# Kernel optimization log

Measured on AMD Instinct MI355X. Metric: run time of the kernel, lower is better.

The kernel has to match this reference:

```python
import jax, jax.numpy as jnp
import numpy as np

N_NODES = 100000
N_EDGES = 1600000
IN_C, HID_C, OUT_C = 128, 128, 64


def setup_inputs() -> dict:
    key = jax.random.key(0)
    ks = jax.random.split(key, 6)
    x = jax.random.normal(ks[0], (N_NODES, IN_C), dtype=jnp.float32)
    edge_index = jax.random.randint(ks[1], (2, N_EDGES), 0, N_NODES)
    W1 = jax.random.normal(ks[2], (IN_C, HID_C), dtype=jnp.float32) * (1.0 / np.sqrt(IN_C))
    b1 = jnp.zeros((HID_C,), dtype=jnp.float32)
    W2 = jax.random.normal(ks[3], (HID_C, OUT_C), dtype=jnp.float32) * (1.0 / np.sqrt(HID_C))
    b2 = jnp.zeros((OUT_C,), dtype=jnp.float32)
    return {"x": x, "edge_index": edge_index, "W1": W1, "b1": b1, "W2": W2, "b2": b2}


def gcn_conv(x, W, b, src, dst):
    # PyG GCNConv: D^{-1/2} (A + I) D^{-1/2} X W + b, with self-loops handled
    # analytically (no explicit self-loop edges materialized).
    h = x @ W                                             # [N, d_out]
    ones = jnp.ones(src.shape[0], dtype=h.dtype)
    deg = jax.ops.segment_sum(ones, dst, num_segments=N_NODES) + 1.0  # +1 self-loop
    dinv = jax.lax.rsqrt(deg)                             # deg >= 1, safe
    norm = dinv[src] * dinv[dst]                          # [E]
    msg = h[src] * norm[:, None]                          # gather + scale  [E, d_out]
    agg = jax.ops.segment_sum(msg, dst, num_segments=N_NODES)
    agg = agg + h * (dinv * dinv)[:, None]                # self-loop contribution
    return agg + b


def reference(x, edge_index, W1, b1, W2, b2):
    src, dst = edge_index[0], edge_index[1]
    h = jax.nn.relu(gcn_conv(x, W1, b1, src, dst))
    # dropout is identity in eval mode
    out = gcn_conv(h, W2, b2, src, dst)
    return out
```

## Files before the change

kernel.cpp:

```cpp
#include <hip/hip_runtime.h>

#define N_NODESC 100000
#define N_EDGESC 1600000
#define NB_BUCKETS 391
#define BUCKET_CAP 5120
#define CHUNK_A 2048
#define NBKT_BLOCKS ((N_EDGESC + CHUNK_A - 1) / CHUNK_A)

typedef __attribute__((ext_vector_type(4))) float floatx4;
typedef __attribute__((ext_vector_type(8))) short shortx8;

__device__ __forceinline__ unsigned short f32_to_bf16_rne(float f) {
    unsigned int u = __float_as_uint(f);
    unsigned int r = u + 0x7fffu + ((u >> 16) & 1u);
    return (unsigned short)(r >> 16);
}
__device__ __forceinline__ float bf16_to_f32(unsigned short h) {
    return __uint_as_float(((unsigned int)h) << 16);
}
__device__ __forceinline__ float bflo(unsigned int u) { return __uint_as_float(u << 16); }
__device__ __forceinline__ float bfhi(unsigned int u) { return __uint_as_float(u & 0xffff0000u); }
__device__ __forceinline__ unsigned int pack2bf(float a, float b) {
    return ((unsigned int)f32_to_bf16_rne(b) << 16) | (unsigned int)f32_to_bf16_rne(a);
}

__global__ __launch_bounds__(256) void k_wfrag_all(const float* __restrict__ W1,
        const float* __restrict__ W2,
        unsigned short* __restrict__ w1hi, unsigned short* __restrict__ w1lo,
        unsigned short* __restrict__ w2hi, unsigned short* __restrict__ w2lo,
        int* __restrict__ gcur) {
    int t = threadIdx.x;
    if (blockIdx.x == 0)
        for (int i = t; i < NB_BUCKETS; i += 256) gcur[i] = i * BUCKET_CAP;
    int idx = blockIdx.x * 256 + t;
    float f;
    int k, col, C, o;
    unsigned short *phi, *plo;
    if (idx < 16384) {
        k = idx >> 7; col = idx & 127; C = 8;
        f = W1[idx]; phi = w1hi; plo = w1lo;
    } else {
        int idx2 = idx - 16384;
        k = idx2 >> 6; col = idx2 & 63; C = 4;
        f = W2[idx2]; phi = w2hi; plo = w2lo;
    }
    unsigned short hi = f32_to_bf16_rne(f);
    unsigned short lo = f32_to_bf16_rne(f - bf16_to_f32(hi));
    int kc = k >> 5, q = (k >> 3) & 3, j = k & 7;
    int c = col >> 4, n = col & 15;
    o = (((kc * C + c) * 4 + q) * 16 + n) * 8 + j;
    phi[o] = hi; plo[o] = lo;
}

__global__ __launch_bounds__(256) void k_fusedA(const float* __restrict__ x,
        const unsigned short* __restrict__ w1hi, const unsigned short* __restrict__ w1lo,
        const int* __restrict__ src, const int* __restrict__ dst,
        int* __restrict__ gcur, unsigned int* __restrict__ tmp,
        unsigned short* __restrict__ H) {
    __shared__ __align__(16) float etile[4][16][132];
    if (blockIdx.x < NBKT_BLOCKS) {
        int* hist = (int*)etile;
        int t = threadIdx.x;
        for (int i = t; i < NB_BUCKETS; i += 256) hist[i] = 0;
        __syncthreads();
        int base = blockIdx.x * CHUNK_A;
        int end = min(base + CHUNK_A, N_EDGESC);
        for (int e = base + t; e < end; e += 256)
            atomicAdd(&hist[dst[e] >> 8], 1);
        __syncthreads();
        for (int i = t; i < NB_BUCKETS; i += 256) {
            int c = hist[i];
            hist[i] = (c > 0) ? atomicAdd(&gcur[i], c) : 0;
        }
        __syncthreads();
        for (int e = base + t; e < end; e += 256) {
            int d = dst[e];
            int pos = atomicAdd(&hist[d >> 8], 1);
            tmp[pos] = ((unsigned int)src[e] << 8) | (unsigned int)(d & 255);
        }
        return;
    }
    int wv = threadIdx.x >> 6, lane = threadIdx.x & 63;
    int n16 = lane & 15, q = lane >> 4;
    int rowBase = (blockIdx.x - NBKT_BLOCKS) * 128 + wv * 32;
    floatx4 acc[2][8];
#pragma unroll
    for (int m = 0; m < 2; ++m)
#pragma unroll
        for (int c = 0; c < 8; ++c) acc[m][c] = (floatx4){0.f, 0.f, 0.f, 0.f};

    const shortx8* whi8 = (const shortx8*)w1hi;
    const shortx8* wlo8 = (const shortx8*)w1lo;

    for (int kc = 0; kc < 4; ++kc) {
        shortx8 ahi[2], alo[2];
#pragma unroll
        for (int m = 0; m < 2; ++m) {
            int r = rowBase + m * 16 + n16;
            if (r >= N_NODESC) r = N_NODESC - 1;
            const float* xp = &x[(size_t)r * 128 + kc * 32 + q * 8];
            floatx4 x0 = *(const floatx4*)xp;
            floatx4 x1 = *(const floatx4*)(xp + 4);
#pragma unroll
            for (int jj = 0; jj < 4; ++jj) {
                unsigned short h0 = f32_to_bf16_rne(x0[jj]);
                ahi[m][jj] = (short)h0;
                alo[m][jj] = (short)f32_to_bf16_rne(x0[jj] - bf16_to_f32(h0));
                unsigned short h1 = f32_to_bf16_rne(x1[jj]);
                ahi[m][jj + 4] = (short)h1;
                alo[m][jj + 4] = (short)f32_to_bf16_rne(x1[jj] - bf16_to_f32(h1));
            }
        }
#pragma unroll
        for (int c = 0; c < 8; ++c) {
            int fo = (kc * 8 + c) * 64 + lane;
            shortx8 bhi = whi8[fo];
            shortx8 blo = wlo8[fo];
#pragma unroll
            for (int m = 0; m < 2; ++m) {
                acc[m][c] = __builtin_amdgcn_mfma_f32_16x16x32_bf16(ahi[m], bhi, acc[m][c], 0, 0, 0);
                acc[m][c] = __builtin_amdgcn_mfma_f32_16x16x32_bf16(alo[m], bhi, acc[m][c], 0, 0, 0);
                acc[m][c] = __builtin_amdgcn_mfma_f32_16x16x32_bf16(ahi[m], blo, acc[m][c], 0, 0, 0);
            }
        }
    }
#pragma unroll
    for (int m = 0; m < 2; ++m) {
        __builtin_amdgcn_wave_barrier();
#pragma unroll
        for (int c = 0; c < 8; ++c)
#pragma unroll
            for (int reg = 0; reg < 4; ++reg)
                etile[wv][q * 4 + reg][c * 16 + n16] = acc[m][c][reg];
        asm volatile("s_waitcnt lgkmcnt(0)" ::: "memory");
        __builtin_amdgcn_wave_barrier();
        int row = lane >> 2, cb = lane & 3;
        int r = rowBase + m * 16 + row;
        if (r < N_NODESC) {
            unsigned int po[16];
#pragma unroll
            for (int i = 0; i < 8; ++i) {
                floatx4 v = *(const floatx4*)&etile[wv][row][cb * 32 + i * 4];
                po[i * 2 + 0] = pack2bf(v[0], v[1]);
                po[i * 2 + 1] = pack2bf(v[2], v[3]);
            }
            unsigned int* op = (unsigned int*)&H[(size_t)r * 128 + cb * 32];
#pragma unroll
            for (int i = 0; i < 4; ++i)
                *(uint4*)(op + i * 4) = *(uint4*)&po[i * 4];
        }
        asm volatile("s_waitcnt lgkmcnt(0)" ::: "memory");
        __builtin_amdgcn_wave_barrier();
    }
}

__global__ __launch_bounds__(1024) void k_place(const unsigned int* __restrict__ tmp,
        const int* __restrict__ gcur,
        int* __restrict__ swsrc, int* __restrict__ deg,
        int* __restrict__ row_ptr, float* __restrict__ dinv) {
    __shared__ unsigned int eb[BUCKET_CAP];
    __shared__ int hist[256], scan[256], lcur[256];
    int b = blockIdx.x, t = threadIdx.x;
    int start = b * BUCKET_CAP;
    int cnt = gcur[b] - start;
    if (t < 256) hist[t] = 0;
    for (int i = t; i < cnt; i += 1024) eb[i] = tmp[start + i];
    __syncthreads();
    for (int i = t; i < cnt; i += 1024)
        atomicAdd(&hist[eb[i] & 255u], 1);
    __syncthreads();
    int own = (t < 256) ? hist[t] : 0;
    if (t < 256) scan[t] = own;
    __syncthreads();
    for (int off = 1; off < 256; off <<= 1) {
        int add = (t >= off && t < 256) ? scan[t - off] : 0;
        __syncthreads();
        if (t < 256) scan[t] += add;
        __syncthreads();
    }
    if (t < 256) {
        int rp = start + scan[t] - own;
        lcur[t] = rp;
        int node = (b << 8) + t;
        if (node < N_NODESC) {
            deg[node] = own;
            row_ptr[node] = rp;
            dinv[node] = rsqrtf((float)own + 1.0f);
        }
    }
    __syncthreads();
    for (int i = t; i < cnt; i += 1024) {
        unsigned int v = eb[i];
        int pos = atomicAdd(&lcur[v & 255u], 1);
        swsrc[pos] = (int)(v >> 8);
    }
}

__global__ __launch_bounds__(256) void k_agg_gemm(const unsigned short* __restrict__ Hb,
        const int* __restrict__ swsrc, const int* __restrict__ row_ptr,
        const int* __restrict__ deg, const float* __restrict__ dinv,
        const float* __restrict__ bias,
        const unsigned short* __restrict__ w2hi, const unsigned short* __restrict__ w2lo,
        unsigned short* __restrict__ H2) {
    __shared__ __align__(16) unsigned int lds_h[16][64];
    int wv = threadIdx.x >> 6, lane = threadIdx.x & 63;
    int g = lane >> 4, l16 = lane & 15;
    int nb = blockIdx.x * 16;

#pragma unroll
    for (int i = 0; i < 4; ++i) {
        int nt = wv * 4 + i;
        int node = nb + nt;
        int start = row_ptr[node];
        int end = start + deg[node];
        float acc[8] = {0.f, 0.f, 0.f, 0.f, 0.f, 0.f, 0.f, 0.f};
        int j = start + g;
        for (; j + 4 < end; j += 8) {
            int s0 = swsrc[j];
            int s1 = swsrc[j + 4];
            float dv0 = dinv[s0];
            float dv1 = dinv[s1];
            uint4 v0 = *(const uint4*)(Hb + (size_t)s0 * 128 + l16 * 8);
            uint4 v1 = *(const uint4*)(Hb + (size_t)s1 * 128 + l16 * 8);
            acc[0] += dv0 * bflo(v0.x) + dv1 * bflo(v1.x);
            acc[1] += dv0 * bfhi(v0.x) + dv1 * bfhi(v1.x);
            acc[2] += dv0 * bflo(v0.y) + dv1 * bflo(v1.y);
            acc[3] += dv0 * bfhi(v0.y) + dv1 * bfhi(v1.y);
            acc[4] += dv0 * bflo(v0.z) + dv1 * bflo(v1.z);
            acc[5] += dv0 * bfhi(v0.z) + dv1 * bfhi(v1.z);
            acc[6] += dv0 * bflo(v0.w) + dv1 * bflo(v1.w);
            acc[7] += dv0 * bfhi(v0.w) + dv1 * bfhi(v1.w);
        }
        if (j < end) {
            int s0 = swsrc[j];
            float dv0 = dinv[s0];
            uint4 v0 = *(const uint4*)(Hb + (size_t)s0 * 128 + l16 * 8);
            acc[0] += dv0 * bflo(v0.x); acc[1] += dv0 * bfhi(v0.x);
            acc[2] += dv0 * bflo(v0.y); acc[3] += dv0 * bfhi(v0.y);
            acc[4] += dv0 * bflo(v0.z); acc[5] += dv0 * bfhi(v0.z);
            acc[6] += dv0 * bflo(v0.w); acc[7] += dv0 * bfhi(v0.w);
        }
#pragma unroll
        for (int k = 0; k < 8; ++k) {
            acc[k] += __shfl_xor(acc[k], 16);
            acc[k] += __shfl_xor(acc[k], 32);
        }
        if (g == 0) {
            float dv = dinv[node];
            uint4 sv = *(const uint4*)(Hb + (size_t)node * 128 + l16 * 8);
            floatx4 b0 = *(const floatx4*)&bias[l16 * 8];
            floatx4 b1 = *(const floatx4*)&bias[l16 * 8 + 4];
            float e0 = dv * (acc[0] + dv * bflo(sv.x)) + b0[0];
            float e1 = dv * (acc[1] + dv * bfhi(sv.x)) + b0[1];
            float e2 = dv * (acc[2] + dv * bflo(sv.y)) + b0[2];
            float e3 = dv * (acc[3] + dv * bfhi(sv.y)) + b0[3];
            float e4 = dv * (acc[4] + dv * bflo(sv.z)) + b1[0];
            float e5 = dv * (acc[5] + dv * bfhi(sv.z)) + b1[1];
            float e6 = dv * (acc[6] + dv * bflo(sv.w)) + b1[2];
            float e7 = dv * (acc[7] + dv * bfhi(sv.w)) + b1[3];
            uint4 o;
            o.x = pack2bf(fmaxf(e0, 0.f), fmaxf(e1, 0.f));
            o.y = pack2bf(fmaxf(e2, 0.f), fmaxf(e3, 0.f));
            o.z = pack2bf(fmaxf(e4, 0.f), fmaxf(e5, 0.f));
            o.w = pack2bf(fmaxf(e6, 0.f), fmaxf(e7, 0.f));
            int pcol = (l16 * 4) ^ ((nt & 7) * 4);
            *(uint4*)&lds_h[nt][pcol] = o;
        }
    }
    __syncthreads();

    int q = lane >> 4, n16 = lane & 15;
    floatx4 accm = (floatx4){0.f, 0.f, 0.f, 0.f};
    const shortx8* whi8 = (const shortx8*)w2hi;
    const shortx8* wlo8 = (const shortx8*)w2lo;
#pragma unroll
    for (int kc = 0; kc < 4; ++kc) {
        int pcol = (kc * 16 + q * 4) ^ ((n16 & 7) * 4);
        shortx8 ahi = *(const shortx8*)&lds_h[n16][pcol];
        int fo = (kc * 4 + wv) * 64 + lane;
        shortx8 bhi = whi8[fo];
        shortx8 blo = wlo8[fo];
        accm = __builtin_amdgcn_mfma_f32_16x16x32_bf16(ahi, bhi, accm, 0, 0, 0);
        accm = __builtin_amdgcn_mfma_f32_16x16x32_bf16(ahi, blo, accm, 0, 0, 0);
    }
    int crow = (lane >> 4) * 4;
    int ccol = wv * 16 + n16;
#pragma unroll
    for (int reg = 0; reg < 4; ++reg) {
        int r = nb + crow + reg;
        float dv = dinv[r];
        H2[(size_t)r * 64 + ccol] = f32_to_bf16_rne(accm[reg] * dv);
    }
}

__global__ __launch_bounds__(256) void k_agg64(const unsigned short* __restrict__ Hb,
        const int* __restrict__ swsrc, const int* __restrict__ row_ptr,
        const int* __restrict__ deg, const float* __restrict__ dinv,
        const float* __restrict__ bias, float* __restrict__ out) {
    int node = blockIdx.x * 4 + (threadIdx.x >> 6);
    int lane = threadIdx.x & 63;
    int g = lane >> 3, l8 = lane & 7;
    int start = row_ptr[node];
    int end = start + deg[node];
    float acc[8] = {0.f, 0.f, 0.f, 0.f, 0.f, 0.f, 0.f, 0.f};
    int j = start + g;
    for (; j + 8 < end; j += 16) {
        int s0 = swsrc[j];
        int s1 = swsrc[j + 8];
        uint4 v0 = *(const uint4*)(Hb + (size_t)s0 * 64 + l8 * 8);
        uint4 v1 = *(const uint4*)(Hb + (size_t)s1 * 64 + l8 * 8);
        acc[0] += bflo(v0.x) + bflo(v1.x);
        acc[1] += bfhi(v0.x) + bfhi(v1.x);
        acc[2] += bflo(v0.y) + bflo(v1.y);
        acc[3] += bfhi(v0.y) + bfhi(v1.y);
        acc[4] += bflo(v0.z) + bflo(v1.z);
        acc[5] += bfhi(v0.z) + bfhi(v1.z);
        acc[6] += bflo(v0.w) + bflo(v1.w);
        acc[7] += bfhi(v0.w) + bfhi(v1.w);
    }
    if (j < end) {
        int s0 = swsrc[j];
        uint4 v0 = *(const uint4*)(Hb + (size_t)s0 * 64 + l8 * 8);
        acc[0] += bflo(v0.x); acc[1] += bfhi(v0.x);
        acc[2] += bflo(v0.y); acc[3] += bfhi(v0.y);
        acc[4] += bflo(v0.z); acc[5] += bfhi(v0.z);
        acc[6] += bflo(v0.w); acc[7] += bfhi(v0.w);
    }
#pragma unroll
    for (int i = 0; i < 8; ++i) {
        acc[i] += __shfl_xor(acc[i], 8);
        acc[i] += __shfl_xor(acc[i], 16);
        acc[i] += __shfl_xor(acc[i], 32);
    }
    if (g == 0) {
        float dv = dinv[node];
        uint4 sv = *(const uint4*)(Hb + (size_t)node * 64 + l8 * 8);
        floatx4 b0 = *(const floatx4*)&bias[l8 * 8];
        floatx4 b1 = *(const floatx4*)&bias[l8 * 8 + 4];
        floatx4 o0, o1;
        o0[0] = dv * (acc[0] + bflo(sv.x)) + b0[0];
        o0[1] = dv * (acc[1] + bfhi(sv.x)) + b0[1];
        o0[2] = dv * (acc[2] + bflo(sv.y)) + b0[2];
        o0[3] = dv * (acc[3] + bfhi(sv.y)) + b0[3];
        o1[0] = dv * (acc[4] + bflo(sv.z)) + b1[0];
        o1[1] = dv * (acc[5] + bfhi(sv.z)) + b1[1];
        o1[2] = dv * (acc[6] + bflo(sv.w)) + b1[2];
        o1[3] = dv * (acc[7] + bfhi(sv.w)) + b1[3];
        *(floatx4*)&out[(size_t)node * 64 + l8 * 8] = o0;
        *(floatx4*)&out[(size_t)node * 64 + l8 * 8 + 4] = o1;
    }
}

extern "C" void kernel_launch(void* const* d_in, const int* in_sizes, int n_in,
                              void* d_out, int out_size, void* d_ws, size_t ws_size,
                              hipStream_t stream) {
    const float* x  = (const float*)d_in[0];
    const int*   ei = (const int*)d_in[1];
    const float* W1 = (const float*)d_in[2];
    const float* b1 = (const float*)d_in[3];
    const float* W2 = (const float*)d_in[4];
    const float* b2 = (const float*)d_in[5];
    float* out = (float*)d_out;
    const int* src = ei;
    const int* dst = ei + N_EDGESC;

    char* ws = (char*)d_ws;
    size_t off = 0;
    auto alloc = [&](size_t bytes) -> void* {
        off = (off + 255) & ~(size_t)255;
        void* p = ws + off;
        off += bytes;
        return p;
    };
    const size_t CSR_SLOTS = (size_t)NB_BUCKETS * BUCKET_CAP;
    int*   deg     = (int*)  alloc((size_t)N_NODESC * 4);
    float* dinv    = (float*)alloc((size_t)N_NODESC * 4);
    int*   row_ptr = (int*)  alloc((size_t)N_NODESC * 4);
    int*   gcur    = (int*)  alloc(NB_BUCKETS * 4);
    unsigned int* tmp   = (unsigned int*)alloc(CSR_SLOTS * 4);
    int*   swsrc   = (int*)  alloc(CSR_SLOTS * 4);
    unsigned short* w1hi = (unsigned short*)alloc(128 * 128 * 2);
    unsigned short* w1lo = (unsigned short*)alloc(128 * 128 * 2);
    unsigned short* w2hi = (unsigned short*)alloc(128 * 64 * 2);
    unsigned short* w2lo = (unsigned short*)alloc(128 * 64 * 2);
    unsigned short* h1b  = (unsigned short*)alloc((size_t)N_NODESC * 128 * 2);
    unsigned short* h2b  = (unsigned short*)alloc((size_t)N_NODESC * 128 * 2);

    const int nbGemm = (N_NODESC + 127) / 128;

    k_wfrag_all<<<(16384 + 8192) / 256, 256, 0, stream>>>(W1, W2, w1hi, w1lo, w2hi, w2lo, gcur);
    k_fusedA<<<NBKT_BLOCKS + nbGemm, 256, 0, stream>>>(x, w1hi, w1lo, src, dst,
                                                       gcur, tmp, h1b);
    k_place<<<NB_BUCKETS, 1024, 0, stream>>>(tmp, gcur, swsrc, deg, row_ptr, dinv);

    k_agg_gemm<<<N_NODESC / 16, 256, 0, stream>>>(h1b, swsrc, row_ptr, deg, dinv, b1,
                                                  w2hi, w2lo, h2b);
    k_agg64<<<N_NODESC / 4, 256, 0, stream>>>(h2b, swsrc, row_ptr, deg, dinv, b2, out);
}
```

Measured before the change: 289.0 us.

## Split layer-1 aggregation into column slices and separate GEMM2, prescale by dinv

Result: slower. 546.2 us (+89.0%).

```diff
diff --git a/kernel.cpp b/kernel.cpp
--- a/kernel.cpp
+++ b/kernel.cpp
@@ -4,8 +4,7 @@
 #define N_EDGESC 1600000
 #define NB_BUCKETS 391
 #define BUCKET_CAP 5120
-#define CHUNK_A 2048
-#define NBKT_BLOCKS ((N_EDGESC + CHUNK_A - 1) / CHUNK_A)
+#define CHUNK_A 4096
 
 typedef __attribute__((ext_vector_type(4))) float floatx4;
 typedef __attribute__((ext_vector_type(8))) short shortx8;
@@ -52,105 +51,27 @@
     phi[o] = hi; plo[o] = lo;
 }
 
-__global__ __launch_bounds__(256) void k_fusedA(const float* __restrict__ x,
-        const unsigned short* __restrict__ w1hi, const unsigned short* __restrict__ w1lo,
-        const int* __restrict__ src, const int* __restrict__ dst,
-        int* __restrict__ gcur, unsigned int* __restrict__ tmp,
-        unsigned short* __restrict__ H) {
-    __shared__ __align__(16) float etile[4][16][132];
-    if (blockIdx.x < NBKT_BLOCKS) {
-        int* hist = (int*)etile;
-        int t = threadIdx.x;
-        for (int i = t; i < NB_BUCKETS; i += 256) hist[i] = 0;
-        __syncthreads();
-        int base = blockIdx.x * CHUNK_A;
-        int end = min(base + CHUNK_A, N_EDGESC);
-        for (int e = base + t; e < end; e += 256)
-            atomicAdd(&hist[dst[e] >> 8], 1);
-        __syncthreads();
-        for (int i = t; i < NB_BUCKETS; i += 256) {
-            int c = hist[i];
-            hist[i] = (c > 0) ? atomicAdd(&gcur[i], c) : 0;
-        }
-        __syncthreads();
-        for (int e = base + t; e < end; e += 256) {
-            int d = dst[e];
-            int pos = atomicAdd(&hist[d >> 8], 1);
-            tmp[pos] = ((unsigned int)src[e] << 8) | (unsigned int)(d & 255);
-        }
-        return;
-    }
-    int wv = threadIdx.x >> 6, lane = threadIdx.x & 63;
-    int n16 = lane & 15, q = lane >> 4;
-    int rowBase = (blockIdx.x - NBKT_BLOCKS) * 128 + wv * 32;
-    floatx4 acc[2][8];
-#pragma unroll
-    for (int m = 0; m < 2; ++m)
-#pragma unroll
-        for (int c = 0; c < 8; ++c) acc[m][c] = (floatx4){0.f, 0.f, 0.f, 0.f};
-
-    const shortx8* whi8 = (const shortx8*)w1hi;
-    const shortx8* wlo8 = (const shortx8*)w1lo;
-
-    for (int kc = 0; kc < 4; ++kc) {
-        shortx8 ahi[2], alo[2];
-#pragma unroll
-        for (int m = 0; m < 2; ++m) {
-            int r = rowBase + m * 16 + n16;
-            if (r >= N_NODESC) r = N_NODESC - 1;
-            const float* xp = &x[(size_t)r * 128 + kc * 32 + q * 8];
-            floatx4 x0 = *(const floatx4*)xp;
-            floatx4 x1 = *(const floatx4*)(xp + 4);
-#pragma unroll
-            for (int jj = 0; jj < 4; ++jj) {
-                unsigned short h0 = f32_to_bf16_rne(x0[jj]);
-                ahi[m][jj] = (short)h0;
-                alo[m][jj] = (short)f32_to_bf16_rne(x0[jj] - bf16_to_f32(h0));
-                unsigned short h1 = f32_to_bf16_rne(x1[jj]);
-                ahi[m][jj + 4] = (short)h1;
-                alo[m][jj + 4] = (short)f32_to_bf16_rne(x1[jj] - bf16_to_f32(h1));
-            }
-        }
-#pragma unroll
-        for (int c = 0; c < 8; ++c) {
-            int fo = (kc * 8 + c) * 64 + lane;
-            shortx8 bhi = whi8[fo];
-            shortx8 blo = wlo8[fo];
-#pragma unroll
-            for (int m = 0; m < 2; ++m) {
-                acc[m][c] = __builtin_amdgcn_mfma_f32_16x16x32_bf16(ahi[m], bhi, acc[m][c], 0, 0, 0);
-                acc[m][c] = __builtin_amdgcn_mfma_f32_16x16x32_bf16(alo[m], bhi, acc[m][c], 0, 0, 0);
-                acc[m][c] = __builtin_amdgcn_mfma_f32_16x16x32_bf16(ahi[m], blo, acc[m][c], 0, 0, 0);
-            }
-        }
-    }
-#pragma unroll
-    for (int m = 0; m < 2; ++m) {
-        __builtin_amdgcn_wave_barrier();
-#pragma unroll
-        for (int c = 0; c < 8; ++c)
-#pragma unroll
-            for (int reg = 0; reg < 4; ++reg)
-                etile[wv][q * 4 + reg][c * 16 + n16] = acc[m][c][reg];
-        asm volatile("s_waitcnt lgkmcnt(0)" ::: "memory");
-        __builtin_amdgcn_wave_barrier();
-        int row = lane >> 2, cb = lane & 3;
-        int r = rowBase + m * 16 + row;
-        if (r < N_NODESC) {
-            unsigned int po[16];
-#pragma unroll
-            for (int i = 0; i < 8; ++i) {
-                floatx4 v = *(const floatx4*)&etile[wv][row][cb * 32 + i * 4];
-                po[i * 2 + 0] = pack2bf(v[0], v[1]);
-                po[i * 2 + 1] = pack2bf(v[2], v[3]);
-            }
-            unsigned int* op = (unsigned int*)&H[(size_t)r * 128 + cb * 32];
-#pragma unroll
-            for (int i = 0; i < 4; ++i)
-                *(uint4*)(op + i * 4) = *(uint4*)&po[i * 4];
-        }
-        asm volatile("s_waitcnt lgkmcnt(0)" ::: "memory");
-        __builtin_amdgcn_wave_barrier();
+__global__ __launch_bounds__(1024) void k_bucket(const int* __restrict__ src,
+        const int* __restrict__ dst, int* __restrict__ gcur,
+        unsigned int* __restrict__ tmp) {
+    __shared__ int hist[NB_BUCKETS];
+    int t = threadIdx.x;
+    for (int i = t; i < NB_BUCKETS; i += 1024) hist[i] = 0;
+    __syncthreads();
+    int base = blockIdx.x * CHUNK_A;
+    int end = min(base + CHUNK_A, N_EDGESC);
+    for (int e = base + t; e < end; e += 1024)
+        atomicAdd(&hist[dst[e] >> 8], 1);
+    __syncthreads();
+    for (int i = t; i < NB_BUCKETS; i += 1024) {
+        int c = hist[i];
+        hist[i] = (c > 0) ? atomicAdd(&gcur[i], c) : 0;
+    }
+    __syncthreads();
+    for (int e = base + t; e < end; e += 1024) {
+        int d = dst[e];
+        int pos = atomicAdd(&hist[d >> 8], 1);
+        tmp[pos] = ((unsigned int)src[e] << 8) | (unsigned int)(d & 255);
     }
 }
 
@@ -196,100 +117,207 @@
     }
 }
 
-__global__ __launch_bounds__(256) void k_agg_gemm(const unsigned short* __restrict__ Hb,
+__global__ __launch_bounds__(256) void k_gemm1(const float* __restrict__ x,
+        const unsigned short* __restrict__ whi, const unsigned short* __restrict__ wlo,
+        const float* __restrict__ dinv, unsigned short* __restrict__ H1s) {
+    __shared__ __align__(16) float etile[4][16][132];
+    int wv = threadIdx.x >> 6, lane = threadIdx.x & 63;
+    int n16 = lane & 15, q = lane >> 4;
+    int rowBase = blockIdx.x * 128 + wv * 32;
+    floatx4 acc[2][8];
+#pragma unroll
+    for (int m = 0; m < 2; ++m)
+#pragma unroll
+        for (int c = 0; c < 8; ++c) acc[m][c] = (floatx4){0.f, 0.f, 0.f, 0.f};
+
+    const shortx8* whi8 = (const shortx8*)whi;
+    const shortx8* wlo8 = (const shortx8*)wlo;
+
+    for (int kc = 0; kc < 4; ++kc) {
+        shortx8 ahi[2], alo[2];
+#pragma unroll
+        for (int m = 0; m < 2; ++m) {
+            int r = rowBase + m * 16 + n16;
+            if (r >= N_NODESC) r = N_NODESC - 1;
+            const float* xp = &x[(size_t)r * 128 + kc * 32 + q * 8];
+            floatx4 x0 = *(const floatx4*)xp;
+            floatx4 x1 = *(const floatx4*)(xp + 4);
+#pragma unroll
+            for (int jj = 0; jj < 4; ++jj) {
+                unsigned short h0 = f32_to_bf16_rne(x0[jj]);
+                ahi[m][jj] = (short)h0;
+                alo[m][jj] = (short)f32_to_bf16_rne(x0[jj] - bf16_to_f32(h0));
+                unsigned short h1 = f32_to_bf16_rne(x1[jj]);
+                ahi[m][jj + 4] = (short)h1;
+                alo[m][jj + 4] = (short)f32_to_bf16_rne(x1[jj] - bf16_to_f32(h1));
+            }
+        }
+#pragma unroll
+        for (int c = 0; c < 8; ++c) {
+            int fo = (kc * 8 + c) * 64 + lane;
+            shortx8 bhi = whi8[fo];
+            shortx8 blo = wlo8[fo];
+#pragma unroll
+            for (int m = 0; m < 2; ++m) {
+                acc[m][c] = __builtin_amdgcn_mfma_f32_16x16x32_bf16(ahi[m], bhi, acc[m][c], 0, 0, 0);
+                acc[m][c] = __builtin_amdgcn_mfma_f32_16x16x32_bf16(alo[m], bhi, acc[m][c], 0, 0, 0);
+                acc[m][c] = __builtin_amdgcn_mfma_f32_16x16x32_bf16(ahi[m], blo, acc[m][c], 0, 0, 0);
+            }
+        }
+    }
+#pragma unroll
+    for (int m = 0; m < 2; ++m) {
+        __builtin_amdgcn_wave_barrier();
+#pragma unroll
+        for (int c = 0; c < 8; ++c)
+#pragma unroll
+            for (int reg = 0; reg < 4; ++reg)
+                etile[wv][q * 4 + reg][c * 16 + n16] = acc[m][c][reg];
+        asm volatile("s_waitcnt lgkmcnt(0)" ::: "memory");
+        __builtin_amdgcn_wave_barrier();
+        int row = lane >> 2, cb = lane & 3;
+        int r = rowBase + m * 16 + row;
+        if (r < N_NODESC) {
+            float dv = dinv[r];
+            unsigned int po[16];
+#pragma unroll
+            for (int i = 0; i < 8; ++i) {
+                floatx4 v = *(const floatx4*)&etile[wv][row][cb * 32 + i * 4];
+                po[i * 2 + 0] = pack2bf(v[0] * dv, v[1] * dv);
+                po[i * 2 + 1] = pack2bf(v[2] * dv, v[3] * dv);
+            }
+            unsigned short* p0 = &H1s[((size_t)(2 * cb) * N_NODESC + r) * 16];
+            unsigned short* p1 = &H1s[((size_t)(2 * cb + 1) * N_NODESC + r) * 16];
+            *(uint4*)p0 = *(uint4*)&po[0];
+            *(uint4*)(p0 + 8) = *(uint4*)&po[4];
+            *(uint4*)p1 = *(uint4*)&po[8];
+            *(uint4*)(p1 + 8) = *(uint4*)&po[12];
+        }
+        asm volatile("s_waitcnt lgkmcnt(0)" ::: "memory");
+        __builtin_amdgcn_wave_barrier();
+    }
+}
+
+__global__ __launch_bounds__(256) void k_agg_sl(const unsigned short* __restrict__ H1s,
         const int* __restrict__ swsrc, const int* __restrict__ row_ptr,
         const int* __restrict__ deg, const float* __restrict__ dinv,
-        const float* __restrict__ bias,
-        const unsigned short* __restrict__ w2hi, const unsigned short* __restrict__ w2lo,
-        unsigned short* __restrict__ H2) {
-    __shared__ __align__(16) unsigned int lds_h[16][64];
+        const float* __restrict__ b1, unsigned short* __restrict__ H1a) {
+    int s = blockIdx.x & 7;
+    int ng = blockIdx.x >> 3;
     int wv = threadIdx.x >> 6, lane = threadIdx.x & 63;
-    int g = lane >> 4, l16 = lane & 15;
-    int nb = blockIdx.x * 16;
-
+    int eslot = lane >> 1, half = lane & 1;
+    const unsigned short* base = H1s + (size_t)s * N_NODESC * 16;
+    unsigned short* obase = H1a + (size_t)s * N_NODESC * 16;
+    floatx4 bb0 = *(const floatx4*)&b1[s * 16 + half * 8];
+    floatx4 bb1 = *(const floatx4*)&b1[s * 16 + half * 8 + 4];
 #pragma unroll
     for (int i = 0; i < 4; ++i) {
-        int nt = wv * 4 + i;
-        int node = nb + nt;
+        int node = ng * 16 + wv * 4 + i;
         int start = row_ptr[node];
         int end = start + deg[node];
         float acc[8] = {0.f, 0.f, 0.f, 0.f, 0.f, 0.f, 0.f, 0.f};
-        int j = start + g;
-        for (; j + 4 < end; j += 8) {
-            int s0 = swsrc[j];
-            int s1 = swsrc[j + 4];
-            float dv0 = dinv[s0];
-            float dv1 = dinv[s1];
-            uint4 v0 = *(const uint4*)(Hb + (size_t)s0 * 128 + l16 * 8);
-            uint4 v1 = *(const uint4*)(Hb + (size_t)s1 * 128 + l16 * 8);
-            acc[0] += dv0 * bflo(v0.x) + dv1 * bflo(v1.x);
-            acc[1] += dv0 * bfhi(v0.x) + dv1 * bfhi(v1.x);
-            acc[2] += dv0 * bflo(v0.y) + dv1 * bflo(v1.y);
-            acc[3] += dv0 * bfhi(v0.y) + dv1 * bfhi(v1.y);
-            acc[4] += dv0 * bflo(v0.z) + dv1 * bflo(v1.z);
-            acc[5] += dv0 * bfhi(v0.z) + dv1 * bfhi(v1.z);
-            acc[6] += dv0 * bflo(v0.w) + dv1 * bflo(v1.w);
-            acc[7] += dv0 * bfhi(v0.w) + dv1 * bfhi(v1.w);
-        }
-        if (j < end) {
-            int s0 = swsrc[j];
-            float dv0 = dinv[s0];
-            uint4 v0 = *(const uint4*)(Hb + (size_t)s0 * 128 + l16 * 8);
-            acc[0] += dv0 * bflo(v0.x); acc[1] += dv0 * bfhi(v0.x);
-            acc[2] += dv0 * bflo(v0.y); acc[3] += dv0 * bfhi(v0.y);
-            acc[4] += dv0 * bflo(v0.z); acc[5] += dv0 * bfhi(v0.z);
-            acc[6] += dv0 * bflo(v0.w); acc[7] += dv0 * bfhi(v0.w);
+        for (int j = start + eslot; j < end; j += 32) {
+            int sc = swsrc[j];
+            uint4 v = *(const uint4*)(base + (size_t)sc * 16 + half * 8);
+            acc[0] += bflo(v.x); acc[1] += bfhi(v.x);
+            acc[2] += bflo(v.y); acc[3] += bfhi(v.y);
+            acc[4] += bflo(v.z); acc[5] += bfhi(v.z);
+            acc[6] += bflo(v.w); acc[7] += bfhi(v.w);
         }
 #pragma unroll
         for (int k = 0; k < 8; ++k) {
+            acc[k] += __shfl_xor(acc[k], 2);
+            acc[k] += __shfl_xor(acc[k], 4);
+            acc[k] += __shfl_xor(acc[k], 8);
             acc[k] += __shfl_xor(acc[k], 16);
             acc[k] += __shfl_xor(acc[k], 32);
         }
-        if (g == 0) {
+        if (eslot == 0) {
             float dv = dinv[node];
-            uint4 sv = *(const uint4*)(Hb + (size_t)node * 128 + l16 * 8);
-            floatx4 b0 = *(const floatx4*)&bias[l16 * 8];
-            floatx4 b1 = *(const floatx4*)&bias[l16 * 8 + 4];
-            float e0 = dv * (acc[0] + dv * bflo(sv.x)) + b0[0];
-            float e1 = dv * (acc[1] + dv * bfhi(sv.x)) + b0[1];
-            float e2 = dv * (acc[2] + dv * bflo(sv.y)) + b0[2];
-            float e3 = dv * (acc[3] + dv * bfhi(sv.y)) + b0[3];
-            float e4 = dv * (acc[4] + dv * bflo(sv.z)) + b1[0];
-            float e5 = dv * (acc[5] + dv * bfhi(sv.z)) + b1[1];
-            float e6 = dv * (acc[6] + dv * bflo(sv.w)) + b1[2];
-            float e7 = dv * (acc[7] + dv * bfhi(sv.w)) + b1[3];
+            uint4 sv = *(const uint4*)(base + (size_t)node * 16 + half * 8);
+            float e0 = dv * (acc[0] + bflo(sv.x)) + bb0[0];
+            float e1 = dv * (acc[1] + bfhi(sv.x)) + bb0[1];
+            float e2 = dv * (acc[2] + bflo(sv.y)) + bb0[2];
+            float e3 = dv * (acc[3] + bfhi(sv.y)) + bb0[3];
+            float e4 = dv * (acc[4] + bflo(sv.z)) + bb1[0];
+            float e5 = dv * (acc[5] + bfhi(sv.z)) + bb1[1];
+            float e6 = dv * (acc[6] + bflo(sv.w)) + bb1[2];
+            float e7 = dv * (acc[7] + bfhi(sv.w)) + bb1[3];
             uint4 o;
             o.x = pack2bf(fmaxf(e0, 0.f), fmaxf(e1, 0.f));
             o.y = pack2bf(fmaxf(e2, 0.f), fmaxf(e3, 0.f));
             o.z = pack2bf(fmaxf(e4, 0.f), fmaxf(e5, 0.f));
             o.w = pack2bf(fmaxf(e6, 0.f), fmaxf(e7, 0.f));
-            int pcol = (l16 * 4) ^ ((nt & 7) * 4);
-            *(uint4*)&lds_h[nt][pcol] = o;
-        }
-    }
-    __syncthreads();
-
-    int q = lane >> 4, n16 = lane & 15;
-    floatx4 accm = (floatx4){0.f, 0.f, 0.f, 0.f};
-    const shortx8* whi8 = (const shortx8*)w2hi;
-    const shortx8* wlo8 = (const shortx8*)w2lo;
-#pragma unroll
+            *(uint4*)(obase + (size_t)node * 16 + half * 8) = o;
+        }
+    }
+}
+
+__global__ __launch_bounds__(256) void k_gemm2(const unsigned short* __restrict__ H1a,
+        const unsigned short* __restrict__ whi, const unsigned short* __restrict__ wlo,
+        const float* __restrict__ dinv, unsigned short* __restrict__ H2) {
+    __shared__ __align__(16) float etile[4][16][68];
+    int wv = threadIdx.x >> 6, lane = threadIdx.x & 63;
+    int n16 = lane & 15, q = lane >> 4;
+    int rowBase = blockIdx.x * 128 + wv * 32;
+    floatx4 acc[2][4];
+#pragma unroll
+    for (int m = 0; m < 2; ++m)
+#pragma unroll
+        for (int c = 0; c < 4; ++c) acc[m][c] = (floatx4){0.f, 0.f, 0.f, 0.f};
+
+    const shortx8* whi8 = (const shortx8*)whi;
+    const shortx8* wlo8 = (const shortx8*)wlo;
+
     for (int kc = 0; kc < 4; ++kc) {
-        int pcol = (kc * 16 + q * 4) ^ ((n16 & 7) * 4);
-        shortx8 ahi = *(const shortx8*)&lds_h[n16][pcol];
-        int fo = (kc * 4 + wv) * 64 + lane;
-        shortx8 bhi = whi8[fo];
-        shortx8 blo = wlo8[fo];
-        accm = __builtin_amdgcn_mfma_f32_16x16x32_bf16(ahi, bhi, accm, 0, 0, 0);
-        accm = __builtin_amdgcn_mfma_f32_16x16x32_bf16(ahi, blo, accm, 0, 0, 0);
-    }
-    int crow = (lane >> 4) * 4;
-    int ccol = wv * 16 + n16;
-#pragma unroll
-    for (int reg = 0; reg < 4; ++reg) {
-        int r = nb + crow + reg;
-        float dv = dinv[r];
-        H2[(size_t)r * 64 + ccol] = f32_to_bf16_rne(accm[reg] * dv);
+        shortx8 ahi[2];
+        int g8 = kc * 4 + q;
+#pragma unroll
+        for (int m = 0; m < 2; ++m) {
+            int r = rowBase + m * 16 + n16;
+            if (r >= N_NODESC) r = N_NODESC - 1;
+            const unsigned short* xp = H1a + ((size_t)(g8 >> 1) * N_NODESC + r) * 16 + (g8 & 1) * 8;
+            ahi[m] = *(const shortx8*)xp;
+        }
+#pragma unroll
+        for (int c = 0; c < 4; ++c) {
+            int fo = (kc * 4 + c) * 64 + lane;
+            shortx8 bhi = whi8[fo];
+            shortx8 blo = wlo8[fo];
+#pragma unroll
+            for (int m = 0; m < 2; ++m) {
+                acc[m][c] = __builtin_amdgcn_mfma_f32_16x16x32_bf16(ahi[m], bhi, acc[m][c], 0, 0, 0);
+                acc[m][c] = __builtin_amdgcn_mfma_f32_16x16x32_bf16(ahi[m], blo, acc[m][c], 0, 0, 0);
+            }
+        }
+    }
+#pragma unroll
+    for (int m = 0; m < 2; ++m) {
+        __builtin_amdgcn_wave_barrier();
+#pragma unroll
+        for (int c = 0; c < 4; ++c)
+#pragma unroll
+            for (int reg = 0; reg < 4; ++reg)
+                etile[wv][q * 4 + reg][c * 16 + n16] = acc[m][c][reg];
+        asm volatile("s_waitcnt lgkmcnt(0)" ::: "memory");
+        __builtin_amdgcn_wave_barrier();
+        int row = lane >> 2, cb = lane & 3;
+        int r = rowBase + m * 16 + row;
+        if (r < N_NODESC) {
+            float dv = dinv[r];
+            unsigned int po[8];
+#pragma unroll
+            for (int i = 0; i < 4; ++i) {
+                floatx4 v = *(const floatx4*)&etile[wv][row][cb * 16 + i * 4];
+                po[i * 2 + 0] = pack2bf(v[0] * dv, v[1] * dv);
+                po[i * 2 + 1] = pack2bf(v[2] * dv, v[3] * dv);
+            }
+            unsigned int* op = (unsigned int*)&H2[(size_t)r * 64 + cb * 16];
+            *(uint4*)(op) = *(uint4*)&po[0];
+            *(uint4*)(op + 4) = *(uint4*)&po[4];
+        }
+        asm volatile("s_waitcnt lgkmcnt(0)" ::: "memory");
+        __builtin_amdgcn_wave_barrier();
     }
 }
 
@@ -383,17 +411,20 @@
     unsigned short* w1lo = (unsigned short*)alloc(128 * 128 * 2);
     unsigned short* w2hi = (unsigned short*)alloc(128 * 64 * 2);
     unsigned short* w2lo = (unsigned short*)alloc(128 * 64 * 2);
-    unsigned short* h1b  = (unsigned short*)alloc((size_t)N_NODESC * 128 * 2);
-    unsigned short* h2b  = (unsigned short*)alloc((size_t)N_NODESC * 128 * 2);
+    unsigned short* h1s  = (unsigned short*)alloc((size_t)N_NODESC * 128 * 2);
+    unsigned short* h1a  = (unsigned short*)alloc((size_t)N_NODESC * 128 * 2);
+    unsigned short* h2b  = (unsigned short*)alloc((size_t)N_NODESC * 64 * 2);
 
     const int nbGemm = (N_NODESC + 127) / 128;
+    const int nbBkt  = (N_EDGESC + CHUNK_A - 1) / CHUNK_A;
+    const int nbAggSl = (N_NODESC / 16) * 8;
 
     k_wfrag_all<<<(16384 + 8192) / 256, 256, 0, stream>>>(W1, W2, w1hi, w1lo, w2hi, w2lo, gcur);
-    k_fusedA<<<NBKT_BLOCKS + nbGemm, 256, 0, stream>>>(x, w1hi, w1lo, src, dst,
-                                                       gcur, tmp, h1b);
+    k_bucket<<<nbBkt, 1024, 0, stream>>>(src, dst, gcur, tmp);
     k_place<<<NB_BUCKETS, 1024, 0, stream>>>(tmp, gcur, swsrc, deg, row_ptr, dinv);
 
-    k_agg_gemm<<<N_NODESC / 16, 256, 0, stream>>>(h1b, swsrc, row_ptr, deg, dinv, b1,
-                                                  w2hi, w2lo, h2b);
+    k_gemm1<<<nbGemm, 256, 0, stream>>>(x, w1hi, w1lo, dinv, h1s);
+    k_agg_sl<<<nbAggSl, 256, 0, stream>>>(h1s, swsrc, row_ptr, deg, dinv, b1, h1a);
+    k_gemm2<<<nbGemm, 256, 0, stream>>>(h1a, w2hi, w2lo, dinv, h2b);
     k_agg64<<<N_NODESC / 4, 256, 0, stream>>>(h2b, swsrc, row_ptr, deg, dinv, b2, out);
 }
```
